# Kernel optimization log

Hardware: AMD Instinct MI355X
Metric: run time of the kernel (lower is better)

## Reference

```python
import jax, jax.numpy as jnp
import numpy as np

B, S, D, H = 2, 2048, 2048, 16
HD = D // H
EPS = 1e-5


def layernorm(x, scale, shift):
    mean = jnp.mean(x, axis=-1, keepdims=True)
    var = jnp.mean((x - mean) ** 2, axis=-1, keepdims=True)  # unbiased=False
    return scale * (x - mean) / jnp.sqrt(var + EPS) + shift


def gelu_buggy(x):
    # Faithful to source: tanh is applied ONLY to the constant sqrt(2/pi)
    c = jnp.tanh(jnp.sqrt(jnp.asarray(2.0 / jnp.pi, dtype=x.dtype)))
    return 0.5 * x * (1.0 + c * (x + 0.044715 * x ** 3))


def setup_inputs() -> dict:
    key = jax.random.key(0)
    ks = jax.random.split(key, 10)
    sd = 0.02
    return {
        "x": jax.random.normal(ks[0], (B, S, D), dtype=jnp.float32),
        "wq": jax.random.normal(ks[1], (D, D), dtype=jnp.float32) * sd,
        "wk": jax.random.normal(ks[2], (D, D), dtype=jnp.float32) * sd,
        "wv": jax.random.normal(ks[3], (D, D), dtype=jnp.float32) * sd,
        "wo": jax.random.normal(ks[4], (D, D), dtype=jnp.float32) * sd,
        "bo": jnp.zeros((D,), dtype=jnp.float32),
        "w1": jax.random.normal(ks[5], (D, 4 * D), dtype=jnp.float32) * sd,
        "b1": jnp.zeros((4 * D,), dtype=jnp.float32),
        "w2": jax.random.normal(ks[6], (4 * D, D), dtype=jnp.float32) * sd,
        "b2": jnp.zeros((D,), dtype=jnp.float32),
        "ln_scale": jnp.ones((D,), dtype=jnp.float32),
        "ln_shift": jnp.zeros((D,), dtype=jnp.float32),
    }


def attention(h, wq, wk, wv, wo, bo):
    b, s, _ = h.shape
    q = (h @ wq).reshape(b, s, H, HD).transpose(0, 2, 1, 3)  # [b,h,s,hd]
    k = (h @ wk).reshape(b, s, H, HD).transpose(0, 2, 1, 3)
    v = (h @ wv).reshape(b, s, H, HD).transpose(0, 2, 1, 3)
    scores = jnp.einsum('bhqd,bhkd->bhqk', q, k)
    causal = jnp.tril(jnp.ones((s, s), dtype=bool))
    scores = jnp.where(causal, scores, -jnp.inf)
    w = jax.nn.softmax(scores / jnp.sqrt(jnp.asarray(HD, dtype=h.dtype)), axis=-1)
    ctx = jnp.einsum('bhqk,bhkd->bhqd', w, v).transpose(0, 2, 1, 3).reshape(b, s, D)
    return ctx @ wo + bo


def reference(x, wq, wk, wv, wo, bo, w1, b1, w2, b2, ln_scale, ln_shift):
    # NB: source applies ln1 before BOTH sub-blocks (ln2 unused); dropout is identity (p=0 / eval)
    shortcut = x
    h = layernorm(x, ln_scale, ln_shift)
    h = attention(h, wq, wk, wv, wo, bo)
    x = h + shortcut
    shortcut = x
    h = layernorm(x, ln_scale, ln_shift)
    h = gelu_buggy(h @ w1 + b1) @ w2 + b2
    return h + shortcut
```

## Files before the change

### kernel.cpp

```cpp
#include <hip/hip_runtime.h>
#include <hip/hip_bf16.h>
#include <math.h>


typedef short bf16x8 __attribute__((ext_vector_type(8)));
typedef float f32x4 __attribute__((ext_vector_type(4)));
typedef short short4v __attribute__((ext_vector_type(4)));

#define MFMA16x32(a, b, c) __builtin_amdgcn_mfma_f32_16x16x32_bf16((a), (b), (c), 0, 0, 0)

__device__ __forceinline__ short f2bs(float f) {
    unsigned u = __builtin_bit_cast(unsigned, f);
    unsigned r = (u + 0x7FFFu + ((u >> 16) & 1u)) >> 16;
    return (short)(unsigned short)r;
}

__device__ __forceinline__ void gload_lds16(const void* g, void* l) {
    __builtin_amdgcn_global_load_lds(
        (const __attribute__((address_space(1))) unsigned int*)g,
        (__attribute__((address_space(3))) unsigned int*)l, 16, 0, 0);
}

__global__ __launch_bounds__(256) void transpose_kernel(const float* __restrict__ in,
                                                        short* __restrict__ out,
                                                        int R, int C) {
    __shared__ float tile[32][33];
    const int tx = threadIdx.x & 31;
    const int ty = threadIdx.x >> 5;
    const int c0 = blockIdx.x * 32;
    const int r0 = blockIdx.y * 32;
#pragma unroll
    for (int i = 0; i < 4; ++i) {
        int r = ty + i * 8;
        tile[r][tx] = in[(size_t)(r0 + r) * C + c0 + tx];
    }
    __syncthreads();
#pragma unroll
    for (int i = 0; i < 4; ++i) {
        int r = ty + i * 8;
        out[(size_t)(c0 + r) * R + r0 + tx] = f2bs(tile[tx][r]);
    }
}

__global__ __launch_bounds__(256) void ln_kernel(const float* __restrict__ x,
                                                 const float* __restrict__ sc,
                                                 const float* __restrict__ sh,
                                                 short* __restrict__ out) {
    const int D = 2048;
    const int row = blockIdx.x;
    const int tid = threadIdx.x;
    __shared__ float red[4];
    const float4* xr = (const float4*)(x + (size_t)row * D);
    float4 v0 = xr[tid];
    float4 v1 = xr[tid + 256];
    float vals0[4] = {v0.x, v0.y, v0.z, v0.w};
    float vals1[4] = {v1.x, v1.y, v1.z, v1.w};

    float s = vals0[0] + vals0[1] + vals0[2] + vals0[3] + vals1[0] + vals1[1] + vals1[2] + vals1[3];
#pragma unroll
    for (int off = 32; off; off >>= 1) s += __shfl_xor(s, off);
    if ((tid & 63) == 0) red[tid >> 6] = s;
    __syncthreads();
    float mean = (red[0] + red[1] + red[2] + red[3]) * (1.0f / 2048.0f);
    __syncthreads();

    float q = 0.0f;
#pragma unroll
    for (int j = 0; j < 4; ++j) {
        float t0 = vals0[j] - mean;
        float t1 = vals1[j] - mean;
        q += t0 * t0 + t1 * t1;
    }
#pragma unroll
    for (int off = 32; off; off >>= 1) q += __shfl_xor(q, off);
    if ((tid & 63) == 0) red[tid >> 6] = q;
    __syncthreads();
    float var = (red[0] + red[1] + red[2] + red[3]) * (1.0f / 2048.0f);
    float inv = rsqrtf(var + 1e-5f);

    const int c0 = tid * 4;
    const int c1 = (tid + 256) * 4;
    short4v o0, o1;
#pragma unroll
    for (int j = 0; j < 4; ++j) {
        o0[j] = f2bs(sc[c0 + j] * ((vals0[j] - mean) * inv) + sh[c0 + j]);
        o1[j] = f2bs(sc[c1 + j] * ((vals1[j] - mean) * inv) + sh[c1 + j]);
    }
    *(short4v*)(out + (size_t)row * D + c0) = o0;
    *(short4v*)(out + (size_t)row * D + c1) = o1;
}

template <int BM, int BN, int EPI>
__global__ __launch_bounds__(512, 2) void gemm8p(const short* __restrict__ Aop,
                                                 const short* __restrict__ Bt,
                                                 int M, int N, int K,
                                                 void* __restrict__ Cout,
                                                 const float* __restrict__ bias,
                                                 const float* __restrict__ res,
                                                 float gconst) {
    constexpr int MF = BM / 32;
    constexpr int NF = BN / 64;
    constexpr int QM = MF / 2, QN = NF / 2;
    constexpr int ASZ = BM * 64;
    constexpr int BSZ = BN * 64;
    extern __shared__ __align__(16) short lds8[];
    short* const A0 = lds8;
    short* const A1 = lds8 + ASZ;
    short* const B0 = lds8 + 2 * ASZ;
    short* const B1 = lds8 + 2 * ASZ + BSZ;

    const int tid = threadIdx.x;
    const int lane = tid & 63;
    const int wid = tid >> 6;
    const int wm = wid >> 2, wn = wid & 3;
    const int l15 = lane & 15, grp = lane >> 4;

    const int gx = gridDim.x;
    int flat = (int)blockIdx.y * gx + (int)blockIdx.x;
    const int cpx = (gx * (int)gridDim.y) >> 3;
    flat = (flat & 7) * cpx + (flat >> 3);
    const int bx = flat % gx, by = flat / gx;
    const long m0 = (long)by * BM, n0 = (long)bx * BN;

    f32x4 zero = {0.f, 0.f, 0.f, 0.f};
    f32x4 acc[MF][NF];
#pragma unroll
    for (int i = 0; i < MF; i++)
#pragma unroll
        for (int j = 0; j < NF; j++) acc[i][j] = zero;
    bf16x8 af[MF][2], bfr[NF][2];

    auto stA = [&](int t, int half, short* dst) {
        const long k0 = (long)t << 6;
#pragma unroll
        for (int j = 0; j < BM / 128; ++j) {
            int c = tid + j * 512;
            int row = c >> 3, sl = (c & 7) ^ (row & 7);
            gload_lds16(Aop + (size_t)(m0 + half * (BM / 2) + row) * K + k0 + sl * 8,
                        dst + (size_t)half * (BM / 2) * 64 + (size_t)c * 8);
        }
    };
    auto stB = [&](int t, int half, short* dst) {
        const long k0 = (long)t << 6;
#pragma unroll
        for (int j = 0; j < BN / 128; ++j) {
            int c = tid + j * 512;
            int row = c >> 3, sl = (c & 7) ^ (row & 7);
            gload_lds16(Bt + (size_t)(n0 + half * (BN / 2) + row) * K + k0 + sl * 8,
                        dst + (size_t)half * (BN / 2) * 64 + (size_t)c * 8);
        }
    };

#define LOADA(qm_, buf_)                                                      \
    _Pragma("unroll") for (int kk = 0; kk < 2; ++kk)                          \
    _Pragma("unroll") for (int mi = 0; mi < QM; ++mi) {                       \
        const int row = wm * (MF * 16) + ((qm_)*QM + mi) * 16 + l15;          \
        af[(qm_)*QM + mi][kk] = *(const bf16x8*)((buf_) + row * 64 +          \
            (((kk * 4 + grp) ^ (row & 7)) * 8));                              \
    }
#define LOADB(qn_, buf_)                                                      \
    _Pragma("unroll") for (int kk = 0; kk < 2; ++kk)                          \
    _Pragma("unroll") for (int ni = 0; ni < QN; ++ni) {                       \
        const int row = wn * (NF * 16) + ((qn_)*QN + ni) * 16 + l15;          \
        bfr[(qn_)*QN + ni][kk] = *(const bf16x8*)((buf_) + row * 64 +         \
            (((kk * 4 + grp) ^ (row & 7)) * 8));                              \
    }
#define QUADM(qm_, qn_)                                                       \
    _Pragma("unroll") for (int kk = 0; kk < 2; ++kk)                          \
    _Pragma("unroll") for (int mi = 0; mi < QM; ++mi)                         \
    _Pragma("unroll") for (int ni = 0; ni < QN; ++ni)                         \
        acc[(qm_)*QM + mi][(qn_)*QN + ni] =                                   \
            MFMA16x32(af[(qm_)*QM + mi][kk], bfr[(qn_)*QN + ni][kk],          \
                      acc[(qm_)*QM + mi][(qn_)*QN + ni]);
#define MIDTAIL(qm_, qn_)                                                     \
    __builtin_amdgcn_s_barrier();                                             \
    asm volatile("s_waitcnt lgkmcnt(0)" ::: "memory");                        \
    __builtin_amdgcn_sched_barrier(0);                                        \
    __builtin_amdgcn_s_setprio(1);                                            \
    QUADM(qm_, qn_);                                                          \
    __builtin_amdgcn_s_setprio(0);                                            \
    __builtin_amdgcn_s_barrier();
#define BARTAIL(qm_, qn_)                                                     \
    __builtin_amdgcn_s_barrier();                                             \
    __builtin_amdgcn_s_setprio(1);                                            \
    QUADM(qm_, qn_);                                                          \
    __builtin_amdgcn_s_setprio(0);                                            \
    __builtin_amdgcn_s_barrier();
#define VMW(lastf)                                                            \
    if (lastf) { asm volatile("s_waitcnt vmcnt(0)" ::: "memory"); }           \
    else if constexpr (BM == 256) { asm volatile("s_waitcnt vmcnt(2)" ::: "memory"); } \
    else { asm volatile("s_waitcnt vmcnt(1)" ::: "memory"); }

    const int nt2 = (K >> 6) >> 1;
    stA(0, 0, A0); stA(0, 1, A0); stB(0, 0, B0); stB(0, 1, B0);
    stA(1, 0, A1);
    VMW(false);
    __builtin_amdgcn_s_barrier();

    for (int i = 0; i < nt2; ++i) {
        const int t = 2 * i;
        const bool last = (i == nt2 - 1);
        stA(t + 1, 1, A1);
        LOADA(0, A0) LOADB(0, B0)
        MIDTAIL(0, 0)
        stB(t + 1, 0, B1);
        LOADA(1, A0)
        MIDTAIL(1, 0)
        stB(t + 1, 1, B1);
        LOADB(1, B0)
        MIDTAIL(0, 1)
        if (!last) stA(t + 2, 0, A0);
        VMW(last);
        BARTAIL(1, 1)
        if (!last) stA(t + 2, 1, A0);
        LOADA(0, A1) LOADB(0, B1)
        MIDTAIL(0, 0)
        if (!last) stB(t + 2, 0, B0);
        LOADA(1, A1)
        MIDTAIL(1, 0)
        if (!last) stB(t + 2, 1, B0);
        LOADB(1, B1)
        MIDTAIL(0, 1)
        if (!last) stA(t + 3, 0, A1);
        VMW(last);
        BARTAIL(1, 1)
    }

#pragma unroll
    for (int mi = 0; mi < MF; mi++) {
        long gr = m0 + wm * (MF * 16) + mi * 16 + grp * 4;
#pragma unroll
        for (int ni = 0; ni < NF; ni++) {
            long gcol = n0 + wn * (NF * 16) + ni * 16 + l15;
#pragma unroll
            for (int r = 0; r < 4; r++) {
                float vv = acc[mi][ni][r];
                long idx = (gr + r) * N + gcol;
                if (EPI == 0) {
                    ((short*)Cout)[idx] = f2bs(vv);
                } else if (EPI == 1) {
                    ((float*)Cout)[idx] = vv + bias[gcol] + res[idx];
                } else {
                    float tv = vv + bias[gcol];
                    float g = 0.5f * tv * (1.0f + gconst * (tv + 0.044715f * tv * tv * tv));
                    ((short*)Cout)[idx] = f2bs(g);
                }
            }
        }
    }
#undef LOADA
#undef LOADB
#undef QUADM
#undef MIDTAIL
#undef BARTAIL
#undef VMW
}

__global__ __launch_bounds__(256) void reshape_k_kernel(const short* __restrict__ qkv,
                                                        short* __restrict__ Kh) {
    size_t idx = ((size_t)blockIdx.x * 256 + threadIdx.x) * 8;
    int d = (int)(idx & 127);
    int s = (int)((idx >> 7) & 2047);
    int bh = (int)(idx >> 18);
    int b = bh >> 4, h = bh & 15;
    const short* src = qkv + (size_t)(b * 2048 + s) * 6144 + 2048 + h * 128 + d;
    *(bf16x8*)(Kh + idx) = *(const bf16x8*)src;
}

__global__ __launch_bounds__(256) void reshape_v_kernel(const short* __restrict__ qkv,
                                                        short* __restrict__ Vt) {
    __shared__ short tile[32][33];
    const int bid = blockIdx.x;
    const int dt = bid & 3, st = (bid >> 2) & 63, bh = bid >> 8;
    const int b = bh >> 4, h = bh & 15;
    const int s0 = st * 32, d0 = dt * 32;
    const int tx = threadIdx.x & 31, ty = threadIdx.x >> 5;
#pragma unroll
    for (int i = 0; i < 4; ++i) {
        int s = ty + i * 8;
        tile[s][tx] = qkv[(size_t)(b * 2048 + s0 + s) * 6144 + 4096 + h * 128 + d0 + tx];
    }
    __syncthreads();
#pragma unroll
    for (int i = 0; i < 4; ++i) {
        int d = ty + i * 8;
        Vt[((size_t)bh * 128 + d0 + d) * 2048 + s0 + tx] = tile[tx][d];
    }
}

__global__ __launch_bounds__(256) void flash3_kernel(const short* __restrict__ qp,
                                                     const short* __restrict__ Kh,
                                                     const short* __restrict__ Vt,
                                                     short* __restrict__ ctx) {
    const int S = 2048, D = 2048, HD = 128, LD = 6144;
    __shared__ __align__(16) short Ks[2][64 * 128];
    __shared__ __align__(16) short Vs[2][64 * 128];
    __shared__ __align__(16) short Ps[4][16 * 64];
    const int tid = threadIdx.x;
    const int lane = tid & 63, wid = tid >> 6;
    const int l15 = lane & 15, grp = lane >> 4;

    int bid = (int)blockIdx.x;
    bid = (bid & 7) * 64 + (bid >> 3);
    const int p = bid & 15, bh = bid >> 4;
    const int b = bh >> 4, h = bh & 15;
    const int qtH = 31 - p;
    const int nH = qtH + 1;
    const float scale = 0.08838834764831845f;
    const float NEGINF = -__builtin_inff();

    const short* Kbase = Kh + (size_t)bh * S * 128;
    const short* Vbase = Vt + (size_t)bh * 128 * S;
    short* Psw = &Ps[wid][0];

    f32x4 zero = {0.f, 0.f, 0.f, 0.f};
    bf16x8 aq[4];
    float m_[4], l_[4];
    f32x4 o[8];

    int qt = qtH;
    int qw = qt * 64 + wid * 16;
    {
        const short* qrow = qp + (size_t)(b * S + qw + l15) * LD + h * HD;
#pragma unroll
        for (int kc = 0; kc < 4; kc++) aq[kc] = *(const bf16x8*)(qrow + kc * 32 + grp * 8);
    }
#pragma unroll
    for (int r = 0; r < 4; r++) { m_[r] = NEGINF; l_[r] = 0.f; }
#pragma unroll
    for (int n = 0; n < 8; n++) o[n] = zero;

#pragma unroll
    for (int j = 0; j < 4; ++j) {
        int c = tid + j * 256;
        int r = c >> 4, sl = c & 15;
        gload_lds16(Kbase + (size_t)r * 128 + ((sl ^ (r & 7)) * 8),
                    Ks[0] + (size_t)(wid * 64 + j * 256) * 8);
    }
#pragma unroll
    for (int j = 0; j < 4; ++j) {
        int c = tid + j * 256;
        int d = c >> 3, sl = c & 7;
        gload_lds16(Vbase + (size_t)d * S + ((sl ^ (d & 7)) * 8),
                    Vs[0] + (size_t)(wid * 64 + j * 256) * 8);
    }
    __syncthreads();

    int cur = 0;
    for (int i = 0; i < 33; ++i) {
        const int kt = (i < nH) ? i : (i - nH);
        const bool lastT = (kt == qt);

        if (i + 1 < 33) {
            const int ktn = (i + 1 < nH) ? (i + 1) : (i + 1 - nH);
            const long kn0 = (long)ktn * 64;
            const short* Kg = Kbase + kn0 * 128;
            const short* Vg = Vbase + kn0;
            short* kd = Ks[cur ^ 1];
            short* vd = Vs[cur ^ 1];
#pragma unroll
            for (int j = 0; j < 4; ++j) {
                int c = tid + j * 256;
                int r = c >> 4, sl = c & 15;
                gload_lds16(Kg + (size_t)r * 128 + ((sl ^ (r & 7)) * 8),
                            kd + (size_t)(wid * 64 + j * 256) * 8);
            }
#pragma unroll
            for (int j = 0; j < 4; ++j) {
                int c = tid + j * 256;
                int d = c >> 3, sl = c & 7;
                gload_lds16(Vg + (size_t)d * S + ((sl ^ (d & 7)) * 8),
                            vd + (size_t)(wid * 64 + j * 256) * 8);
            }
        }

        const short* Kc = Ks[cur];
        const short* Vc = Vs[cur];

        f32x4 s[4] = {zero, zero, zero, zero};
#pragma unroll
        for (int n = 0; n < 4; ++n) {
            int r = n * 16 + l15;
#pragma unroll
            for (int kc = 0; kc < 4; ++kc) {
                bf16x8 kb = *(const bf16x8*)(Kc + r * 128 + (((kc * 4 + grp) ^ (r & 7)) * 8));
                s[n] = MFMA16x32(aq[kc], kb, s[n]);
            }
        }

        float al[4];
#pragma unroll
        for (int r = 0; r < 4; ++r) {
            float v[4];
#pragma unroll
            for (int n = 0; n < 4; ++n) v[n] = s[n][r] * scale;
            if (lastT) {
                int qrel = wid * 16 + grp * 4 + r;
#pragma unroll
                for (int n = 0; n < 4; ++n)
                    if (n * 16 + l15 > qrel) v[n] = NEGINF;
            }
            float mx = fmaxf(fmaxf(v[0], v[1]), fmaxf(v[2], v[3]));
            mx = fmaxf(mx, __shfl_xor(mx, 1));
            mx = fmaxf(mx, __shfl_xor(mx, 2));
            mx = fmaxf(mx, __shfl_xor(mx, 4));
            mx = fmaxf(mx, __shfl_xor(mx, 8));
            float mn = fmaxf(m_[r], mx);
            float sc_ = __expf(m_[r] - mn);
            float rs = 0.f;
            int q = grp * 4 + r;
#pragma unroll
            for (int n = 0; n < 4; ++n) {
                v[n] = __expf(v[n] - mn);
                rs += v[n];
                Psw[q * 64 + (((n * 2 + (l15 >> 3)) ^ (q & 7)) * 8) + (l15 & 7)] = f2bs(v[n]);
            }
            rs += __shfl_xor(rs, 1);
            rs += __shfl_xor(rs, 2);
            rs += __shfl_xor(rs, 4);
            rs += __shfl_xor(rs, 8);
            l_[r] = l_[r] * sc_ + rs;
            m_[r] = mn;
            al[r] = sc_;
        }
#pragma unroll
        for (int n = 0; n < 8; n++) {
            f32x4 t = o[n];
            t[0] *= al[0]; t[1] *= al[1]; t[2] *= al[2]; t[3] *= al[3];
            o[n] = t;
        }

        bf16x8 pa[2];
#pragma unroll
        for (int kc = 0; kc < 2; ++kc)
            pa[kc] = *(const bf16x8*)(Psw + l15 * 64 + (((kc * 4 + grp) ^ (l15 & 7)) * 8));
#pragma unroll
        for (int n = 0; n < 8; ++n) {
            int d = n * 16 + l15;
#pragma unroll
            for (int kc = 0; kc < 2; ++kc) {
                bf16x8 vb = *(const bf16x8*)(Vc + d * 64 + (((kc * 4 + grp) ^ (d & 7)) * 8));
                o[n] = MFMA16x32(pa[kc], vb, o[n]);
            }
        }

        if (lastT) {
            float inv[4];
#pragma unroll
            for (int r = 0; r < 4; ++r) inv[r] = 1.0f / l_[r];
            short* cb_ = ctx + (size_t)(b * S + qw + grp * 4) * D + h * HD + l15;
#pragma unroll
            for (int n = 0; n < 8; ++n)
#pragma unroll
                for (int r = 0; r < 4; ++r)
                    cb_[(size_t)r * D + n * 16] = f2bs(o[n][r] * inv[r]);
            if (i < 32) {
                qt = 31 - qtH;
                qw = qt * 64 + wid * 16;
                const short* qrow = qp + (size_t)(b * S + qw + l15) * LD + h * HD;
#pragma unroll
                for (int kc = 0; kc < 4; kc++) aq[kc] = *(const bf16x8*)(qrow + kc * 32 + grp * 8);
#pragma unroll
                for (int r = 0; r < 4; r++) { m_[r] = NEGINF; l_[r] = 0.f; }
#pragma unroll
                for (int n = 0; n < 8; n++) o[n] = zero;
            }
        }
        __syncthreads();
        cur ^= 1;
    }
}

extern "C" void kernel_launch(void* const* d_in, const int* in_sizes, int n_in,
                              void* d_out, int out_size, void* d_ws, size_t ws_size,
                              hipStream_t stream) {
    const float* x    = (const float*)d_in[0];
    const float* wq   = (const float*)d_in[1];
    const float* wk   = (const float*)d_in[2];
    const float* wv   = (const float*)d_in[3];
    const float* wo   = (const float*)d_in[4];
    const float* bo   = (const float*)d_in[5];
    const float* w1   = (const float*)d_in[6];
    const float* b1   = (const float*)d_in[7];
    const float* w2   = (const float*)d_in[8];
    const float* b2   = (const float*)d_in[9];
    const float* lnsc = (const float*)d_in[10];
    const float* lnsh = (const float*)d_in[11];

    const int B = 2, S = 2048, D = 2048;
    const int M = B * S;
    const int LDS_BIG = 2 * (256 * 64 + 256 * 64) * 2;
    const int LDS_SML = 2 * (128 * 64 + 256 * 64) * 2;

    char* p = (char*)d_ws;
    short* wqkvT = (short*)p; p += (size_t)3 * D * D * 2;
    short* woT   = (short*)p; p += (size_t)D * D * 2;
    short* w1T   = (short*)p; p += (size_t)4 * D * D * 2;
    short* w2T   = (short*)p; p += (size_t)4 * D * D * 2;
    short* lnb   = (short*)p; p += (size_t)M * D * 2;
    short* qkvb  = (short*)p;
    short* h1    = qkvb;
    p += (size_t)M * 3 * D * 2;
    short* ctxb  = (short*)p; p += (size_t)M * D * 2;
    float* x2    = (float*)p; p += (size_t)M * D * 4;

    short* Kh = wqkvT;
    short* Vt = (short*)x2;

    const float gconst = tanhf(sqrtf(2.0f / 3.14159265358979323846f));

    hipFuncSetAttribute((const void*)&gemm8p<256, 256, 0>, hipFuncAttributeMaxDynamicSharedMemorySize, LDS_BIG);
    hipFuncSetAttribute((const void*)&gemm8p<256, 256, 2>, hipFuncAttributeMaxDynamicSharedMemorySize, LDS_BIG);
    hipFuncSetAttribute((const void*)&gemm8p<128, 256, 1>, hipFuncAttributeMaxDynamicSharedMemorySize, LDS_SML);

    dim3 blk(256);
    transpose_kernel<<<dim3(64, 64), blk, 0, stream>>>(wq, wqkvT, D, D);
    transpose_kernel<<<dim3(64, 64), blk, 0, stream>>>(wk, wqkvT + (size_t)D * D, D, D);
    transpose_kernel<<<dim3(64, 64), blk, 0, stream>>>(wv, wqkvT + (size_t)2 * D * D, D, D);
    transpose_kernel<<<dim3(64, 64), blk, 0, stream>>>(wo, woT, D, D);
    transpose_kernel<<<dim3(256, 64), blk, 0, stream>>>(w1, w1T, D, 4 * D);
    transpose_kernel<<<dim3(64, 256), blk, 0, stream>>>(w2, w2T, 4 * D, D);

    ln_kernel<<<dim3(M), blk, 0, stream>>>(x, lnsc, lnsh, lnb);
    gemm8p<256, 256, 0><<<dim3(3 * D / 256, M / 256), dim3(512), LDS_BIG, stream>>>(
        lnb, wqkvT, M, 3 * D, D, qkvb, nullptr, nullptr, 0.f);

    reshape_k_kernel<<<dim3(4096), blk, 0, stream>>>(qkvb, Kh);
    reshape_v_kernel<<<dim3(8192), blk, 0, stream>>>(qkvb, Vt);

    flash3_kernel<<<dim3(512), blk, 0, stream>>>(qkvb, Kh, Vt, ctxb);

    gemm8p<128, 256, 1><<<dim3(D / 256, M / 128), dim3(512), LDS_SML, stream>>>(
        ctxb, woT, M, D, D, x2, bo, x, 0.f);
    ln_kernel<<<dim3(M), blk, 0, stream>>>(x2, lnsc, lnsh, lnb);
    gemm8p<256, 256, 2><<<dim3(4 * D / 256, M / 256), dim3(512), LDS_BIG, stream>>>(
        lnb, w1T, M, 4 * D, D, h1, b1, nullptr, gconst);
    gemm8p<128, 256, 1><<<dim3(D / 256, M / 128), dim3(512), LDS_SML, stream>>>(
        h1, w2T, M, D, 4 * D, (float*)d_out, b2, x2, 0.f);
}
```

Before: 660.7 us.

## Reschedule GEMM global-to-LDS prefetches and waitcnts across the eight-phase loop

Reorders where the global_load_lds stages for the next A and B tiles are issued relative to each compute phase. Each stage is now issued before its phase's barrier, and whole A tiles are prefetched ahead with deeper vmcnt waits. Every phase now waits on lgkmcnt, and sched_barriers pin the ordering. The goal is to hide more global latency behind MFMA work. The cost is more outstanding loads and stricter scheduling, and the vmcnt counts must exactly match the issued loads or the code reads stale LDS.

New measurement: 680.7 us. 1.03x slower.

```diff
diff --git a/kernel.cpp b/kernel.cpp
--- a/kernel.cpp
+++ b/kernel.cpp
@@ -19,6 +19,13 @@
     __builtin_amdgcn_global_load_lds(
         (const __attribute__((address_space(1))) unsigned int*)g,
         (__attribute__((address_space(3))) unsigned int*)l, 16, 0, 0);
+}
+
+template <int N>
+__device__ __forceinline__ void vmw() {
+    if constexpr (N == 0) asm volatile("s_waitcnt vmcnt(0)" ::: "memory");
+    else if constexpr (N == 2) asm volatile("s_waitcnt vmcnt(2)" ::: "memory");
+    else if constexpr (N == 4) asm volatile("s_waitcnt vmcnt(4)" ::: "memory");
 }
 
 __global__ __launch_bounds__(256) void transpose_kernel(const float* __restrict__ in,
@@ -103,6 +110,7 @@
     constexpr int QM = MF / 2, QN = NF / 2;
     constexpr int ASZ = BM * 64;
     constexpr int BSZ = BN * 64;
+    constexpr int V4 = (BM == 256) ? 4 : 2;
     extern __shared__ __align__(16) short lds8[];
     short* const A0 = lds8;
     short* const A1 = lds8 + ASZ;
@@ -172,7 +180,8 @@
         acc[(qm_)*QM + mi][(qn_)*QN + ni] =                                   \
             MFMA16x32(af[(qm_)*QM + mi][kk], bfr[(qn_)*QN + ni][kk],          \
                       acc[(qm_)*QM + mi][(qn_)*QN + ni]);
-#define MIDTAIL(qm_, qn_)                                                     \
+#define PHT(qm_, qn_)                                                         \
+    __builtin_amdgcn_sched_barrier(0);                                        \
     __builtin_amdgcn_s_barrier();                                             \
     asm volatile("s_waitcnt lgkmcnt(0)" ::: "memory");                        \
     __builtin_amdgcn_sched_barrier(0);                                        \
@@ -180,50 +189,42 @@
     QUADM(qm_, qn_);                                                          \
     __builtin_amdgcn_s_setprio(0);                                            \
     __builtin_amdgcn_s_barrier();
-#define BARTAIL(qm_, qn_)                                                     \
-    __builtin_amdgcn_s_barrier();                                             \
-    __builtin_amdgcn_s_setprio(1);                                            \
-    QUADM(qm_, qn_);                                                          \
-    __builtin_amdgcn_s_setprio(0);                                            \
-    __builtin_amdgcn_s_barrier();
-#define VMW(lastf)                                                            \
-    if (lastf) { asm volatile("s_waitcnt vmcnt(0)" ::: "memory"); }           \
-    else if constexpr (BM == 256) { asm volatile("s_waitcnt vmcnt(2)" ::: "memory"); } \
-    else { asm volatile("s_waitcnt vmcnt(1)" ::: "memory"); }
-
-    const int nt2 = (K >> 6) >> 1;
+
+    const int nt = K >> 6;
+    const int nt2 = nt >> 1;
     stA(0, 0, A0); stA(0, 1, A0); stB(0, 0, B0); stB(0, 1, B0);
-    stA(1, 0, A1);
-    VMW(false);
+    stA(1, 0, A1); stA(1, 1, A1);
+    vmw<V4>();
     __builtin_amdgcn_s_barrier();
 
     for (int i = 0; i < nt2; ++i) {
         const int t = 2 * i;
-        const bool last = (i == nt2 - 1);
-        stA(t + 1, 1, A1);
+        const bool haveT2 = (t + 2 < nt);
+        const bool haveT3 = (t + 3 < nt);
         LOADA(0, A0) LOADB(0, B0)
-        MIDTAIL(0, 0)
         stB(t + 1, 0, B1);
+        PHT(0, 0)
         LOADA(1, A0)
-        MIDTAIL(1, 0)
         stB(t + 1, 1, B1);
+        PHT(1, 0)
         LOADB(1, B0)
-        MIDTAIL(0, 1)
-        if (!last) stA(t + 2, 0, A0);
-        VMW(last);
-        BARTAIL(1, 1)
-        if (!last) stA(t + 2, 1, A0);
+        if (haveT2) stA(t + 2, 0, A0);
+        PHT(0, 1)
+        if (haveT2) stA(t + 2, 1, A0);
+        if (haveT2) { vmw<V4>(); } else { vmw<0>(); }
+        PHT(1, 1)
         LOADA(0, A1) LOADB(0, B1)
-        MIDTAIL(0, 0)
-        if (!last) stB(t + 2, 0, B0);
+        if (haveT2) stB(t + 2, 0, B0);
+        PHT(0, 0)
         LOADA(1, A1)
-        MIDTAIL(1, 0)
-        if (!last) stB(t + 2, 1, B0);
+        if (haveT2) stB(t + 2, 1, B0);
+        PHT(1, 0)
         LOADB(1, B1)
-        MIDTAIL(0, 1)
-        if (!last) stA(t + 3, 0, A1);
-        VMW(last);
-        BARTAIL(1, 1)
+        if (haveT3) stA(t + 3, 0, A1);
+        PHT(0, 1)
+        if (haveT3) stA(t + 3, 1, A1);
+        if (haveT2) { vmw<V4>(); }
+        PHT(1, 1)
     }
 
 #pragma unroll
@@ -251,9 +252,7 @@
 #undef LOADA
 #undef LOADB
 #undef QUADM
-#undef MIDTAIL
-#undef BARTAIL
-#undef VMW
+#undef PHT
 }
 
 __global__ __launch_bounds__(256) void reshape_k_kernel(const short* __restrict__ qkv,
```
